# Optimization experiments

Measured on AMD Instinct MI355X. Metric: run time of the kernel, lower is better.

The kernel has to match this reference:

```python
import jax, jax.numpy as jnp
import numpy as np

B, S, I, H = 128, 512, 128, 512  # batch, seq_length(image_height), input_size(image_width), hidden(latent_dim)


def setup_inputs() -> dict:
    key = jax.random.key(0)
    ks = jax.random.split(key, 18)
    scale = 0.05

    def w(k, shape):
        return (jax.random.normal(k, shape, jnp.float32) * scale)

    inp = {"x": jax.random.normal(ks[0], (B, S, I), jnp.float32)}
    idx = 1
    for pre, in_sz in [("en0", I), ("en1", H), ("de0", I), ("de1", H)]:
        inp[f"W_ih_{pre}"] = w(ks[idx], (4 * H, in_sz)); idx += 1
        inp[f"W_hh_{pre}"] = w(ks[idx], (4 * H, H)); idx += 1
        inp[f"b_ih_{pre}"] = w(ks[idx], (4 * H,)); idx += 1
        inp[f"b_hh_{pre}"] = w(ks[idx], (4 * H,)); idx += 1
    inp["W_lin"] = w(ks[17], (I, H))  # nn.Linear(hidden, input, bias=False)
    return inp


def _cell(x, h, c, W_ih, W_hh, b_ih, b_hh):
    # PyTorch LSTM gate order: i, f, g, o
    gates = x @ W_ih.T + h @ W_hh.T + b_ih + b_hh
    i, f, g, o = jnp.split(gates, 4, axis=-1)
    c = jax.nn.sigmoid(f) * c + jax.nn.sigmoid(i) * jnp.tanh(g)
    h = jax.nn.sigmoid(o) * jnp.tanh(c)
    return h, c


def reference(x,
              W_ih_en0, W_hh_en0, b_ih_en0, b_hh_en0,
              W_ih_en1, W_hh_en1, b_ih_en1, b_hh_en1,
              W_ih_de0, W_hh_de0, b_ih_de0, b_hh_de0,
              W_ih_de1, W_hh_de1, b_ih_de1, b_hh_de1,
              W_lin):
    x = x.reshape((B, S, I))
    z = jnp.zeros((B, H), x.dtype)

    # ---- encoder: 2-layer LSTM, keep only final (hidden, cell) ----
    def enc_step(carry, xt):
        h0, c0, h1, c1 = carry
        h0, c0 = _cell(xt, h0, c0, W_ih_en0, W_hh_en0, b_ih_en0, b_hh_en0)
        h1, c1 = _cell(h0, h1, c1, W_ih_en1, W_hh_en1, b_ih_en1, b_hh_en1)
        return (h0, c0, h1, c1), None

    (h0, c0, h1, c1), _ = jax.lax.scan(enc_step, (z, z, z, z), jnp.swapaxes(x, 0, 1))

    # ---- decoder: closed-loop, feeding linear(output) back in ----
    def dec_step(carry, _):
        inp, h0, c0, h1, c1 = carry
        h0, c0 = _cell(inp, h0, c0, W_ih_de0, W_hh_de0, b_ih_de0, b_hh_de0)
        h1, c1 = _cell(h0, h1, c1, W_ih_de1, W_hh_de1, b_ih_de1, b_hh_de1)
        pred = h1 @ W_lin.T  # [B, I]
        return (pred, h0, c0, h1, c1), pred

    inp0 = jnp.zeros((B, I), x.dtype)
    _, preds = jax.lax.scan(dec_step, (inp0, h0, c0, h1, c1), None, length=S)
    return jnp.swapaxes(preds, 0, 1)  # [B, S, I]
```

## Files before the change

kernel.cpp:

```cpp
#include <hip/hip_runtime.h>
#include <hip/hip_fp16.h>


#define DEVINL __device__ __forceinline__

typedef _Float16 f16;
typedef _Float16 f16x8 __attribute__((ext_vector_type(8)));
typedef float    f32x4 __attribute__((ext_vector_type(4)));

constexpr int B = 128, S = 512, I = 128, H = 512, G4 = 4 * H;

constexpr size_t OFF_CNT    = 0;
constexpr size_t OFF_H1DBUF = 32768;
constexpr size_t OFF_C0     = 294912;
constexpr size_t OFF_C1     = 557056;
constexpr size_t OFF_H0ALL  = 819200;
constexpr size_t OFF_DDBUF  = 68059136;
constexpr size_t OFF_H1ST   = 68321280;
constexpr size_t OFF_XF16   = 135430144;
constexpr size_t OFF_WLIN16 = 152207360;
constexpr size_t OFF_BSUM   = 152338432;
constexpr size_t OFF_WEFF   = 152371200;
constexpr size_t ZERO_BYTES = 950272;

constexpr int LDS_L0   = 0;
constexpr int LDS_L1   = 40960;
constexpr int LDS_D0   = 0;
constexpr int LDS_D1   = 65536;
constexpr int LDS_SCR  = 131072;
constexpr int LDS_GB   = 146432;
constexpr int LDS_C0   = 150656;
constexpr int LDS_C1   = 151680;
constexpr int SMEM_BYTES = 152704;

DEVINL void cload(f16x8& r, const f16* p) {
    asm volatile("global_load_dwordx4 %0, %1, off sc0 sc1" : "=v"(r) : "v"(p));
}
DEVINL void ncload(f16x8& r, const f16* p) {
    asm volatile("global_load_dwordx4 %0, %1, off" : "=v"(r) : "v"(p));
}
DEVINL void cstore_h(f16* p, unsigned v) {
    asm volatile("global_store_short %0, %1, off sc0 sc1" :: "v"(p), "v"(v));
}
DEVINL void drain_vm() {
    asm volatile("s_waitcnt vmcnt(0)" ::: "memory");
    __builtin_amdgcn_sched_barrier(0);
}

__global__ void prep_kernel(const float* __restrict__ x,
                            const float* b0a, const float* b0b,
                            const float* b1a, const float* b1b,
                            const float* b2a, const float* b2b,
                            const float* b3a, const float* b3b,
                            const float* __restrict__ wlin, char* ws) {
    f16*   xf = (f16*)(ws + OFF_XF16);
    f16*   wl = (f16*)(ws + OFF_WLIN16);
    float* bs = (float*)(ws + OFF_BSUM);
    int tid = blockIdx.x * blockDim.x + threadIdx.x;
    int nth = gridDim.x * blockDim.x;
    for (int idx = tid; idx < S * B * I; idx += nth) {
        int i = idx & 127, b = (idx >> 7) & 127, t = idx >> 14;
        xf[idx] = (f16)x[((size_t)b * S + t) * I + i];
    }
    for (int idx = tid; idx < I * H; idx += nth) wl[idx] = (f16)wlin[idx];
    for (int idx = tid; idx < G4; idx += nth) {
        bs[idx]          = b0a[idx] + b0b[idx];
        bs[G4 + idx]     = b1a[idx] + b1b[idx];
        bs[2 * G4 + idx] = b2a[idx] + b2b[idx];
        bs[3 * G4 + idx] = b3a[idx] + b3b[idx];
    }
}

__global__ void weff_kernel(const float* __restrict__ wih_de0,
                            const float* __restrict__ wlin, char* ws) {
    float* weff = (float*)(ws + OFF_WEFF);
    int e  = blockIdx.x * 256 + threadIdx.x;
    int gc = e >> 9, k = e & 511;
    float acc = 0.f;
    for (int i = 0; i < I; ++i) acc += wih_de0[gc * I + i] * wlin[i * H + k];
    weff[e] = acc;
}

struct PParams {
    const float *wih0, *whh0, *wih1, *whh1, *whh2, *wih3, *whh3;
    char* ws;
};

DEVINL void wait2(unsigned* a, unsigned* b) {
    if (threadIdx.x == 0 && a)
        while (__hip_atomic_load(a, __ATOMIC_RELAXED, __HIP_MEMORY_SCOPE_AGENT) < 64u) {}
    if (threadIdx.x == 64 && b)
        while (__hip_atomic_load(b, __ATOMIC_RELAXED, __HIP_MEMORY_SCOPE_AGENT) < 64u) {}
    __syncthreads();
}

DEVINL void arrive(unsigned* c) {
    asm volatile("s_waitcnt vmcnt(0)" ::: "memory");
    __syncthreads();
    if (threadIdx.x == 0)
        __hip_atomic_fetch_add(c, 1u, __ATOMIC_RELAXED, __HIP_MEMORY_SCOPE_AGENT);
}

template <int K, int SPLIT>
DEVINL void fill_w(f16* ldsW, const float* __restrict__ matA,
                   const float* __restrict__ matB, int j0) {
    for (int idx = threadIdx.x; idx < 32 * K; idx += 512) {
        int c = idx / K, k = idx - c * K;
        int gcol = ((c >> 3) << 9) + j0 + (c & 7);
        float w = (k < SPLIT) ? matA[(size_t)gcol * SPLIT + k]
                              : matB[(size_t)gcol * (K - SPLIT) + (k - SPLIT)];
        int nt = c >> 4, lane = (((k >> 3) & 3) << 4) | (c & 15);
        int ks = k >> 5, j = k & 7;
        ldsW[(((size_t)nt * (K / 32) + ks) * 64 + lane) * 8 + j] = (f16)w;
    }
}

template <int K, int SPLIT, bool NCA>
DEVINL void lstm_round(const f16* __restrict__ actA, int strA,
                       const f16* __restrict__ actB, int strB, bool skipA,
                       const f16* __restrict__ ldsW, float biasN0, float biasN1,
                       float* scr, float* gb, float* c_lds,
                       f16* __restrict__ hdst, int m_idx, int j0) {
    const int tid = threadIdx.x;
    const int wv = tid >> 6, lane = tid & 63;
    const int m_t = wv >> 2, k_q = wv & 3;
    const int row = m_idx * 32 + m_t * 16 + (lane & 15);
    const int kk0 = (lane >> 4) * 8;
    constexpr int KS = K / 32;
    constexpr int SQ = KS / 4;
    const int ks0 = k_q * SQ;
    const f16* pa = actA + (size_t)row * strA + kk0;
    const f16* pb = actB + (size_t)row * strB + kk0 - SPLIT;

    f16x8 areg[SQ];
#pragma unroll
    for (int s = 0; s < SQ; ++s) {
        int kbase = (ks0 + s) * 32;
        if (kbase < SPLIT) {
            if (skipA) {
#pragma unroll
                for (int q = 0; q < 8; ++q) areg[s][q] = (f16)0;
            } else if (NCA) ncload(areg[s], pa + kbase);
            else            cload(areg[s], pa + kbase);
        } else cload(areg[s], pb + kbase);
    }
    drain_vm();

    f32x4 acc0 = (k_q == 0) ? (f32x4){biasN0, biasN0, biasN0, biasN0}
                            : (f32x4){0.f, 0.f, 0.f, 0.f};
    f32x4 acc1 = (k_q == 0) ? (f32x4){biasN1, biasN1, biasN1, biasN1}
                            : (f32x4){0.f, 0.f, 0.f, 0.f};
#pragma unroll
    for (int s = 0; s < SQ; ++s) {
        int ks = ks0 + s;
        f16x8 b0 = *(const f16x8*)(ldsW + (size_t)(ks * 64 + lane) * 8);
        f16x8 b1 = *(const f16x8*)(ldsW + (size_t)((KS + ks) * 64 + lane) * 8);
        acc0 = __builtin_amdgcn_mfma_f32_16x16x32_f16(areg[s], b0, acc0, 0, 0, 0);
        acc1 = __builtin_amdgcn_mfma_f32_16x16x32_f16(areg[s], b1, acc1, 0, 0, 0);
    }

    const int col = lane & 15, r0 = (lane >> 4) * 4;
    if (k_q) {
        *(f32x4*)(scr + ((m_t * 2 + 0) * 3 + (k_q - 1)) * 320 + col * 20 + r0) = acc0;
        *(f32x4*)(scr + ((m_t * 2 + 1) * 3 + (k_q - 1)) * 320 + col * 20 + r0) = acc1;
    }
    __syncthreads();
    if (k_q == 0) {
#pragma unroll
        for (int part = 0; part < 3; ++part) {
            acc0 += *(const f32x4*)(scr + ((m_t * 2 + 0) * 3 + part) * 320 + col * 20 + r0);
            acc1 += *(const f32x4*)(scr + ((m_t * 2 + 1) * 3 + part) * 320 + col * 20 + r0);
        }
#pragma unroll
        for (int i = 0; i < 4; ++i) {
            gb[(m_t * 16 + r0 + i) * 33 + col]      = acc0[i];
            gb[(m_t * 16 + r0 + i) * 33 + 16 + col] = acc1[i];
        }
    }
    __syncthreads();
    if (tid < 256) {
        int r = tid >> 3, jj = tid & 7;
        const float* grow = gb + r * 33;
        float gi = grow[jj], gf = grow[8 + jj], gg = grow[16 + jj], go = grow[24 + jj];
        float si = 1.f / (1.f + __expf(-gi));
        float sf = 1.f / (1.f + __expf(-gf));
        float so = 1.f / (1.f + __expf(-go));
        float tg = tanhf(gg);
        float cn = sf * c_lds[tid] + si * tg;
        c_lds[tid] = cn;
        union { f16 h; unsigned short u; } cvt;
        cvt.h = (f16)(so * tanhf(cn));
        cstore_h(hdst + (size_t)(m_idx * 32 + r) * H + j0 + jj, (unsigned)cvt.u);
    }
}

__global__ void __launch_bounds__(512, 1) lstm_persistent(PParams p) {
    extern __shared__ char smem[];
    char* ws = p.ws;
    unsigned* cnt = (unsigned*)(ws + OFF_CNT);
    f16*   h1db = (f16*)(ws + OFF_H1DBUF);
    f16*   h0all= (f16*)(ws + OFF_H0ALL);
    f16*   ddb  = (f16*)(ws + OFF_DDBUF);
    f16*   h1st = (f16*)(ws + OFF_H1ST);
    const f16*   xf   = (const f16*)(ws + OFF_XF16);
    const float* bs   = (const float*)(ws + OFF_BSUM);
    const float* weff = (const float*)(ws + OFF_WEFF);

    const int wg = blockIdx.x;
    const int m_idx = wg >> 6;
    const int n_idx = wg & 63;
    const int j0 = n_idx * 8;
    const int lane = threadIdx.x & 63;
    int c0col = lane & 15, c1col = 16 + (lane & 15);
    int g0 = ((c0col >> 3) << 9) + j0 + (c0col & 7);
    int g1 = ((c1col >> 3) << 9) + j0 + (c1col & 7);
    float b0n0 = bs[g0],          b0n1 = bs[g1];
    float b1n0 = bs[G4 + g0],     b1n1 = bs[G4 + g1];
    float b2n0 = bs[2 * G4 + g0], b2n1 = bs[2 * G4 + g1];
    float b3n0 = bs[3 * G4 + g0], b3n1 = bs[3 * G4 + g1];

    f16* ldsL0 = (f16*)(smem + LDS_L0);
    f16* ldsL1 = (f16*)(smem + LDS_L1);
    f16* ldsD0 = (f16*)(smem + LDS_D0);
    f16* ldsD1 = (f16*)(smem + LDS_D1);
    float* scr = (float*)(smem + LDS_SCR);
    float* gb  = (float*)(smem + LDS_GB);
    float* c0l = (float*)(smem + LDS_C0);
    float* c1l = (float*)(smem + LDS_C1);

    unsigned* cL0 = cnt;
    unsigned* cL1 = cnt + 512 * 4;
    unsigned* cD0 = cnt + 2 * 512 * 4;
    unsigned* cD1 = cnt + 3 * 512 * 4;

    if (threadIdx.x < 256) { c0l[threadIdx.x] = 0.f; c1l[threadIdx.x] = 0.f; }
    fill_w<640, 128>(ldsL0, p.wih0, p.whh0, j0);
    fill_w<1024, 512>(ldsL1, p.wih1, p.whh1, j0);
    __syncthreads();

    const int LAG = 3;
    for (int r = 0; r < 512 + LAG; ++r) {
        if (r < 512) {
            int t = r;
            wait2(t > 0 ? &cL0[(t - 1) * 4 + m_idx] : nullptr, nullptr);
            lstm_round<640, 128, true>(xf + (size_t)t * B * I, I,
                                       h0all + (size_t)t * B * H, H, false,
                                       ldsL0, b0n0, b0n1, scr, gb, c0l,
                                       h0all + (size_t)(t + 1) * B * H, m_idx, j0);
            arrive(&cL0[t * 4 + m_idx]);
        }
        if (r >= LAG) {
            int t = r - LAG;
            wait2(&cL0[t * 4 + m_idx],
                  t > 0 ? &cL1[(t - 1) * 4 + m_idx] : nullptr);
            lstm_round<1024, 512, false>(h0all + (size_t)(t + 1) * B * H, H,
                                         h1db + (size_t)((t - 1) & 1) * B * H, H, false,
                                         ldsL1, b1n0, b1n1, scr, gb, c1l,
                                         h1db + (size_t)(t & 1) * B * H, m_idx, j0);
            arrive(&cL1[t * 4 + m_idx]);
        }
    }

    __syncthreads();
    fill_w<1024, 512>(ldsD0, weff, p.whh2, j0);
    fill_w<1024, 512>(ldsD1, p.wih3, p.whh3, j0);
    __syncthreads();

    for (int t = 0; t < 512; ++t) {
        if (t == 0) wait2(&cL1[511 * 4 + m_idx], nullptr);
        else        wait2(&cD0[(t - 1) * 4 + m_idx], &cD1[(t - 1) * 4 + m_idx]);
        lstm_round<1024, 512, false>(
            t == 0 ? (h1db + (size_t)1 * B * H) : (h1st + (size_t)(t - 1) * B * H), H,
            t == 0 ? (h0all + (size_t)512 * B * H) : (ddb + (size_t)((t - 1) & 1) * B * H), H,
            t == 0,
            ldsD0, b2n0, b2n1, scr, gb, c0l,
            ddb + (size_t)(t & 1) * B * H, m_idx, j0);
        arrive(&cD0[t * 4 + m_idx]);

        wait2(&cD0[t * 4 + m_idx],
              t > 0 ? &cD1[(t - 1) * 4 + m_idx] : nullptr);
        lstm_round<1024, 512, false>(
            ddb + (size_t)(t & 1) * B * H, H,
            t == 0 ? (h1db + (size_t)1 * B * H) : (h1st + (size_t)(t - 1) * B * H), H,
            false,
            ldsD1, b3n0, b3n1, scr, gb, c1l,
            h1st + (size_t)t * B * H, m_idx, j0);
        arrive(&cD1[t * 4 + m_idx]);
    }
}

__global__ void __launch_bounds__(256) pred_kernel(const f16* __restrict__ h1s,
                                                   const f16* __restrict__ wl,
                                                   float* __restrict__ out) {
    int wg = blockIdx.x;
    int wv = threadIdx.x >> 6, lane = threadIdx.x & 63;
    int m0 = wg * 64 + wv * 16;
    int arow = m0 + (lane & 15);
    int kk0 = (lane >> 4) * 8;
    f32x4 acc[8];
#pragma unroll
    for (int n = 0; n < 8; ++n) acc[n] = (f32x4){0.f, 0.f, 0.f, 0.f};
#pragma unroll
    for (int ks = 0; ks < 16; ++ks) {
        f16x8 a = *(const f16x8*)(h1s + (size_t)arow * H + ks * 32 + kk0);
#pragma unroll
        for (int n = 0; n < 8; ++n) {
            f16x8 b = *(const f16x8*)(wl + (size_t)(n * 16 + (lane & 15)) * H + ks * 32 + kk0);
            acc[n] = __builtin_amdgcn_mfma_f32_16x16x32_f16(a, b, acc[n], 0, 0, 0);
        }
    }
    int col = lane & 15, r0 = (lane >> 4) * 4;
#pragma unroll
    for (int n = 0; n < 8; ++n)
#pragma unroll
        for (int i = 0; i < 4; ++i) {
            int m = m0 + r0 + i;
            int t = m >> 7, b = m & 127;
            out[((size_t)b * S + t) * I + n * 16 + col] = acc[n][i];
        }
}

extern "C" void kernel_launch(void* const* d_in, const int* in_sizes, int n_in,
                              void* d_out, int out_size, void* d_ws, size_t ws_size,
                              hipStream_t stream) {
    (void)in_sizes; (void)n_in; (void)out_size; (void)ws_size;
    const float* x        = (const float*)d_in[0];
    const float* wih_en0  = (const float*)d_in[1];
    const float* whh_en0  = (const float*)d_in[2];
    const float* bih_en0  = (const float*)d_in[3];
    const float* bhh_en0  = (const float*)d_in[4];
    const float* wih_en1  = (const float*)d_in[5];
    const float* whh_en1  = (const float*)d_in[6];
    const float* bih_en1  = (const float*)d_in[7];
    const float* bhh_en1  = (const float*)d_in[8];
    const float* wih_de0  = (const float*)d_in[9];
    const float* whh_de0  = (const float*)d_in[10];
    const float* bih_de0  = (const float*)d_in[11];
    const float* bhh_de0  = (const float*)d_in[12];
    const float* wih_de1  = (const float*)d_in[13];
    const float* whh_de1  = (const float*)d_in[14];
    const float* bih_de1  = (const float*)d_in[15];
    const float* bhh_de1  = (const float*)d_in[16];
    const float* wlin     = (const float*)d_in[17];
    char* ws = (char*)d_ws;

    hipMemsetAsync(ws, 0, ZERO_BYTES, stream);
    prep_kernel<<<2048, 256, 0, stream>>>(x, bih_en0, bhh_en0, bih_en1, bhh_en1,
                                          bih_de0, bhh_de0, bih_de1, bhh_de1,
                                          wlin, ws);
    weff_kernel<<<4096, 256, 0, stream>>>(wih_de0, wlin, ws);

    hipFuncSetAttribute((const void*)lstm_persistent,
                        hipFuncAttributeMaxDynamicSharedMemorySize, SMEM_BYTES);
    PParams p{wih_en0, whh_en0, wih_en1, whh_en1, whh_de0, wih_de1, whh_de1, ws};
    void* args[] = {&p};
    hipLaunchCooperativeKernel((const void*)lstm_persistent, dim3(256), dim3(512),
                               args, SMEM_BYTES, stream);

    pred_kernel<<<1024, 256, 0, stream>>>((const f16*)(ws + OFF_H1ST),
                                          (const f16*)(ws + OFF_WLIN16),
                                          (float*)d_out);
}
```

Measured before the change: 13.26 ms.

## Split encoder layers across dedicated workgroups and use per-block flag barriers

The encoder is restructured so the first 128 workgroups run layer 0 and the other 128 run layer 1 concurrently, each covering 64 rows with a 4x2 wave split, instead of every workgroup interleaving both layers with a fixed lag. The shared atomic counters are replaced by per-workgroup monotonic flags that a whole wavefront polls and checks with __all, and arrival becomes a plain store. Encoder cell states are handed to the decoder through global memory. Some activation loads switch from cache-bypassing asm to ordinary loads where the data was written earlier. This aims to cut serialisation and synchronisation latency in the recurrence, but it relies on those ordinary loads not returning stale cached data.

```diff
diff --git a/kernel.cpp b/kernel.cpp
--- a/kernel.cpp
+++ b/kernel.cpp
@@ -10,10 +10,10 @@
 
 constexpr int B = 128, S = 512, I = 128, H = 512, G4 = 4 * H;
 
-constexpr size_t OFF_CNT    = 0;
+constexpr size_t OFF_FLAGS  = 0;
 constexpr size_t OFF_H1DBUF = 32768;
-constexpr size_t OFF_C0     = 294912;
-constexpr size_t OFF_C1     = 557056;
+constexpr size_t OFF_C0G    = 294912;
+constexpr size_t OFF_C1G    = 557056;
 constexpr size_t OFF_H0ALL  = 819200;
 constexpr size_t OFF_DDBUF  = 68059136;
 constexpr size_t OFF_H1ST   = 68321280;
@@ -23,24 +23,25 @@
 constexpr size_t OFF_WEFF   = 152371200;
 constexpr size_t ZERO_BYTES = 950272;
 
-constexpr int LDS_L0   = 0;
-constexpr int LDS_L1   = 40960;
-constexpr int LDS_D0   = 0;
-constexpr int LDS_D1   = 65536;
+constexpr int LDS_W0   = 0;
+constexpr int LDS_W1   = 65536;
 constexpr int LDS_SCR  = 131072;
 constexpr int LDS_GB   = 146432;
-constexpr int LDS_C0   = 150656;
-constexpr int LDS_C1   = 151680;
-constexpr int SMEM_BYTES = 152704;
+constexpr int LDS_CA   = 154880;
+constexpr int LDS_CB   = 156928;
+constexpr int SMEM_BYTES = 158976;
 
 DEVINL void cload(f16x8& r, const f16* p) {
     asm volatile("global_load_dwordx4 %0, %1, off sc0 sc1" : "=v"(r) : "v"(p));
 }
-DEVINL void ncload(f16x8& r, const f16* p) {
-    asm volatile("global_load_dwordx4 %0, %1, off" : "=v"(r) : "v"(p));
+DEVINL void cload_f32(float& r, const float* p) {
+    asm volatile("global_load_dword %0, %1, off sc0 sc1" : "=v"(r) : "v"(p));
 }
 DEVINL void cstore_h(f16* p, unsigned v) {
     asm volatile("global_store_short %0, %1, off sc0 sc1" :: "v"(p), "v"(v));
+}
+DEVINL void cstore_f32(float* p, float v) {
+    asm volatile("global_store_dword %0, %1, off sc0 sc1" :: "v"(p), "v"(v));
 }
 DEVINL void drain_vm() {
     asm volatile("s_waitcnt vmcnt(0)" ::: "memory");
@@ -86,19 +87,30 @@
     char* ws;
 };
 
-DEVINL void wait2(unsigned* a, unsigned* b) {
-    if (threadIdx.x == 0 && a)
-        while (__hip_atomic_load(a, __ATOMIC_RELAXED, __HIP_MEMORY_SCOPE_AGENT) < 64u) {}
-    if (threadIdx.x == 64 && b)
-        while (__hip_atomic_load(b, __ATOMIC_RELAXED, __HIP_MEMORY_SCOPE_AGENT) < 64u) {}
-    __syncthreads();
-}
-
-DEVINL void arrive(unsigned* c) {
-    asm volatile("s_waitcnt vmcnt(0)" ::: "memory");
+DEVINL void waitA(const unsigned* f, unsigned tgt) {
+    if (f && threadIdx.x < 64) {
+        unsigned v;
+        do {
+            v = __hip_atomic_load(f + (threadIdx.x & 63),
+                                  __ATOMIC_RELAXED, __HIP_MEMORY_SCOPE_AGENT);
+        } while (!__all((int)(v >= tgt)));
+    }
+}
+DEVINL void waitB(const unsigned* f, unsigned tgt) {
+    if (f && threadIdx.x >= 64 && threadIdx.x < 128) {
+        unsigned v;
+        do {
+            v = __hip_atomic_load(f + (threadIdx.x & 63),
+                                  __ATOMIC_RELAXED, __HIP_MEMORY_SCOPE_AGENT);
+        } while (!__all((int)(v >= tgt)));
+    }
+}
+
+DEVINL void arrive(unsigned* f, unsigned val) {
+    drain_vm();
     __syncthreads();
     if (threadIdx.x == 0)
-        __hip_atomic_fetch_add(c, 1u, __ATOMIC_RELAXED, __HIP_MEMORY_SCOPE_AGENT);
+        __hip_atomic_store(f, val, __ATOMIC_RELAXED, __HIP_MEMORY_SCOPE_AGENT);
 }
 
 template <int K, int SPLIT>
@@ -115,20 +127,20 @@
     }
 }
 
-template <int K, int SPLIT, bool NCA>
+template <int K, int SPLIT, int MT, int KP, int AMODE, int BMODE>
 DEVINL void lstm_round(const f16* __restrict__ actA, int strA,
                        const f16* __restrict__ actB, int strB, bool skipA,
                        const f16* __restrict__ ldsW, float biasN0, float biasN1,
                        float* scr, float* gb, float* c_lds,
-                       f16* __restrict__ hdst, int m_idx, int j0) {
+                       f16* __restrict__ hdst, int row0, int j0) {
     const int tid = threadIdx.x;
     const int wv = tid >> 6, lane = tid & 63;
-    const int m_t = wv >> 2, k_q = wv & 3;
-    const int row = m_idx * 32 + m_t * 16 + (lane & 15);
+    const int m_t = wv / KP, k_p = wv % KP;
+    const int row = row0 + m_t * 16 + (lane & 15);
     const int kk0 = (lane >> 4) * 8;
     constexpr int KS = K / 32;
-    constexpr int SQ = KS / 4;
-    const int ks0 = k_q * SQ;
+    constexpr int SQ = KS / KP;
+    const int ks0 = k_p * SQ;
     const f16* pa = actA + (size_t)row * strA + kk0;
     const f16* pb = actB + (size_t)row * strB + kk0 - SPLIT;
 
@@ -140,15 +152,18 @@
             if (skipA) {
 #pragma unroll
                 for (int q = 0; q < 8; ++q) areg[s][q] = (f16)0;
-            } else if (NCA) ncload(areg[s], pa + kbase);
-            else            cload(areg[s], pa + kbase);
-        } else cload(areg[s], pb + kbase);
+            } else if (AMODE == 0) areg[s] = *(const f16x8*)(pa + kbase);
+            else                   cload(areg[s], pa + kbase);
+        } else {
+            if (BMODE == 0) areg[s] = *(const f16x8*)(pb + kbase);
+            else            cload(areg[s], pb + kbase);
+        }
     }
     drain_vm();
 
-    f32x4 acc0 = (k_q == 0) ? (f32x4){biasN0, biasN0, biasN0, biasN0}
+    f32x4 acc0 = (k_p == 0) ? (f32x4){biasN0, biasN0, biasN0, biasN0}
                             : (f32x4){0.f, 0.f, 0.f, 0.f};
-    f32x4 acc1 = (k_q == 0) ? (f32x4){biasN1, biasN1, biasN1, biasN1}
+    f32x4 acc1 = (k_p == 0) ? (f32x4){biasN1, biasN1, biasN1, biasN1}
                             : (f32x4){0.f, 0.f, 0.f, 0.f};
 #pragma unroll
     for (int s = 0; s < SQ; ++s) {
@@ -160,16 +175,16 @@
     }
 
     const int col = lane & 15, r0 = (lane >> 4) * 4;
-    if (k_q) {
-        *(f32x4*)(scr + ((m_t * 2 + 0) * 3 + (k_q - 1)) * 320 + col * 20 + r0) = acc0;
-        *(f32x4*)(scr + ((m_t * 2 + 1) * 3 + (k_q - 1)) * 320 + col * 20 + r0) = acc1;
-    }
-    __syncthreads();
-    if (k_q == 0) {
-#pragma unroll
-        for (int part = 0; part < 3; ++part) {
-            acc0 += *(const f32x4*)(scr + ((m_t * 2 + 0) * 3 + part) * 320 + col * 20 + r0);
-            acc1 += *(const f32x4*)(scr + ((m_t * 2 + 1) * 3 + part) * 320 + col * 20 + r0);
+    if (k_p) {
+        *(f32x4*)(scr + ((m_t * 2 + 0) * (KP - 1) + (k_p - 1)) * 320 + col * 20 + r0) = acc0;
+        *(f32x4*)(scr + ((m_t * 2 + 1) * (KP - 1) + (k_p - 1)) * 320 + col * 20 + r0) = acc1;
+    }
+    __syncthreads();
+    if (k_p == 0) {
+#pragma unroll
+        for (int part = 0; part < KP - 1; ++part) {
+            acc0 += *(const f32x4*)(scr + ((m_t * 2 + 0) * (KP - 1) + part) * 320 + col * 20 + r0);
+            acc1 += *(const f32x4*)(scr + ((m_t * 2 + 1) * (KP - 1) + part) * 320 + col * 20 + r0);
         }
 #pragma unroll
         for (int i = 0; i < 4; ++i) {
@@ -178,7 +193,7 @@
         }
     }
     __syncthreads();
-    if (tid < 256) {
+    if (tid < MT * 128) {
         int r = tid >> 3, jj = tid & 7;
         const float* grow = gb + r * 33;
         float gi = grow[jj], gf = grow[8 + jj], gg = grow[16 + jj], go = grow[24 + jj];
@@ -190,15 +205,21 @@
         c_lds[tid] = cn;
         union { f16 h; unsigned short u; } cvt;
         cvt.h = (f16)(so * tanhf(cn));
-        cstore_h(hdst + (size_t)(m_idx * 32 + r) * H + j0 + jj, (unsigned)cvt.u);
+        cstore_h(hdst + (size_t)(row0 + r) * H + j0 + jj, (unsigned)cvt.u);
     }
 }
 
 __global__ void __launch_bounds__(512, 1) lstm_persistent(PParams p) {
     extern __shared__ char smem[];
     char* ws = p.ws;
-    unsigned* cnt = (unsigned*)(ws + OFF_CNT);
+    unsigned* flg = (unsigned*)(ws + OFF_FLAGS);
+    unsigned* fL0 = flg;
+    unsigned* fL1 = flg + 128;
+    unsigned* fD0 = flg + 256;
+    unsigned* fD1 = flg + 512;
     f16*   h1db = (f16*)(ws + OFF_H1DBUF);
+    float* c0g  = (float*)(ws + OFF_C0G);
+    float* c1g  = (float*)(ws + OFF_C1G);
     f16*   h0all= (f16*)(ws + OFF_H0ALL);
     f16*   ddb  = (f16*)(ws + OFF_DDBUF);
     f16*   h1st = (f16*)(ws + OFF_H1ST);
@@ -207,10 +228,13 @@
     const float* weff = (const float*)(ws + OFF_WEFF);
 
     const int wg = blockIdx.x;
-    const int m_idx = wg >> 6;
+    const bool isL0 = wg < 128;
+    const int mh = (wg & 127) >> 6;
+    const int m  = wg >> 6;
     const int n_idx = wg & 63;
     const int j0 = n_idx * 8;
-    const int lane = threadIdx.x & 63;
+    const int tid = threadIdx.x, lane = tid & 63;
+
     int c0col = lane & 15, c1col = 16 + (lane & 15);
     int g0 = ((c0col >> 3) << 9) + j0 + (c0col & 7);
     int g1 = ((c1col >> 3) << 9) + j0 + (c1col & 7);
@@ -219,73 +243,98 @@
     float b2n0 = bs[2 * G4 + g0], b2n1 = bs[2 * G4 + g1];
     float b3n0 = bs[3 * G4 + g0], b3n1 = bs[3 * G4 + g1];
 
-    f16* ldsL0 = (f16*)(smem + LDS_L0);
-    f16* ldsL1 = (f16*)(smem + LDS_L1);
-    f16* ldsD0 = (f16*)(smem + LDS_D0);
-    f16* ldsD1 = (f16*)(smem + LDS_D1);
+    f16* ldsW0 = (f16*)(smem + LDS_W0);
+    f16* ldsW1 = (f16*)(smem + LDS_W1);
     float* scr = (float*)(smem + LDS_SCR);
     float* gb  = (float*)(smem + LDS_GB);
-    float* c0l = (float*)(smem + LDS_C0);
-    float* c1l = (float*)(smem + LDS_C1);
-
-    unsigned* cL0 = cnt;
-    unsigned* cL1 = cnt + 512 * 4;
-    unsigned* cD0 = cnt + 2 * 512 * 4;
-    unsigned* cD1 = cnt + 3 * 512 * 4;
-
-    if (threadIdx.x < 256) { c0l[threadIdx.x] = 0.f; c1l[threadIdx.x] = 0.f; }
-    fill_w<640, 128>(ldsL0, p.wih0, p.whh0, j0);
-    fill_w<1024, 512>(ldsL1, p.wih1, p.whh1, j0);
-    __syncthreads();
-
-    const int LAG = 3;
-    for (int r = 0; r < 512 + LAG; ++r) {
-        if (r < 512) {
-            int t = r;
-            wait2(t > 0 ? &cL0[(t - 1) * 4 + m_idx] : nullptr, nullptr);
-            lstm_round<640, 128, true>(xf + (size_t)t * B * I, I,
-                                       h0all + (size_t)t * B * H, H, false,
-                                       ldsL0, b0n0, b0n1, scr, gb, c0l,
-                                       h0all + (size_t)(t + 1) * B * H, m_idx, j0);
-            arrive(&cL0[t * 4 + m_idx]);
-        }
-        if (r >= LAG) {
-            int t = r - LAG;
-            wait2(&cL0[t * 4 + m_idx],
-                  t > 0 ? &cL1[(t - 1) * 4 + m_idx] : nullptr);
-            lstm_round<1024, 512, false>(h0all + (size_t)(t + 1) * B * H, H,
-                                         h1db + (size_t)((t - 1) & 1) * B * H, H, false,
-                                         ldsL1, b1n0, b1n1, scr, gb, c1l,
-                                         h1db + (size_t)(t & 1) * B * H, m_idx, j0);
-            arrive(&cL1[t * 4 + m_idx]);
-        }
-    }
-
-    __syncthreads();
-    fill_w<1024, 512>(ldsD0, weff, p.whh2, j0);
-    fill_w<1024, 512>(ldsD1, p.wih3, p.whh3, j0);
+    float* cA  = (float*)(smem + LDS_CA);
+    float* cB  = (float*)(smem + LDS_CB);
+
+    if (isL0) {
+        fill_w<640, 128>(ldsW0, p.wih0, p.whh0, j0);
+        cA[tid] = 0.f;
+        __syncthreads();
+        for (int t = 0; t < 512; ++t) {
+            waitA(t > 0 ? &fL0[mh * 64] : nullptr, (unsigned)t);
+            __syncthreads();
+            lstm_round<640, 128, 4, 2, 0, 0>(
+                xf + (size_t)t * B * I, I,
+                h0all + (size_t)t * B * H, H, false,
+                ldsW0, b0n0, b0n1, scr, gb, cA,
+                h0all + (size_t)(t + 1) * B * H, mh * 64, j0);
+            if (t == 511)
+                cstore_f32(&c0g[(size_t)(mh * 64 + (tid >> 3)) * H + j0 + (tid & 7)], cA[tid]);
+            arrive(&fL0[mh * 64 + n_idx], (unsigned)(t + 1));
+        }
+    } else {
+        fill_w<1024, 512>(ldsW0, p.wih1, p.whh1, j0);
+        cA[tid] = 0.f;
+        __syncthreads();
+        for (int t = 0; t < 512; ++t) {
+            waitA(&fL0[mh * 64], (unsigned)(t + 1));
+            waitB(t > 0 ? &fL1[mh * 64] : nullptr, (unsigned)t);
+            __syncthreads();
+            lstm_round<1024, 512, 4, 2, 0, 1>(
+                h0all + (size_t)(t + 1) * B * H, H,
+                h1db + (size_t)((t - 1) & 1) * B * H, H, false,
+                ldsW0, b1n0, b1n1, scr, gb, cA,
+                h1db + (size_t)(t & 1) * B * H, mh * 64, j0);
+            if (t == 511)
+                cstore_f32(&c1g[(size_t)(mh * 64 + (tid >> 3)) * H + j0 + (tid & 7)], cA[tid]);
+            arrive(&fL1[mh * 64 + n_idx], (unsigned)(t + 1));
+        }
+    }
+
+    __syncthreads();
+    fill_w<1024, 512>(ldsW0, weff, p.whh2, j0);
+    fill_w<1024, 512>(ldsW1, p.wih3, p.whh3, j0);
+    waitA(&fL0[(m >> 1) * 64], 512u);
+    waitB(&fL1[(m >> 1) * 64], 512u);
+    __syncthreads();
+    {
+        int r = (tid & 255) >> 3, jj = tid & 7;
+        float v;
+        cload_f32(v, (tid < 256 ? c0g : c1g) + (size_t)(m * 32 + r) * H + j0 + jj);
+        asm volatile("s_waitcnt vmcnt(0)" ::: "memory");
+        (tid < 256 ? cA : cB)[tid & 255] = v;
+    }
     __syncthreads();
 
     for (int t = 0; t < 512; ++t) {
-        if (t == 0) wait2(&cL1[511 * 4 + m_idx], nullptr);
-        else        wait2(&cD0[(t - 1) * 4 + m_idx], &cD1[(t - 1) * 4 + m_idx]);
-        lstm_round<1024, 512, false>(
-            t == 0 ? (h1db + (size_t)1 * B * H) : (h1st + (size_t)(t - 1) * B * H), H,
-            t == 0 ? (h0all + (size_t)512 * B * H) : (ddb + (size_t)((t - 1) & 1) * B * H), H,
-            t == 0,
-            ldsD0, b2n0, b2n1, scr, gb, c0l,
-            ddb + (size_t)(t & 1) * B * H, m_idx, j0);
-        arrive(&cD0[t * 4 + m_idx]);
-
-        wait2(&cD0[t * 4 + m_idx],
-              t > 0 ? &cD1[(t - 1) * 4 + m_idx] : nullptr);
-        lstm_round<1024, 512, false>(
-            ddb + (size_t)(t & 1) * B * H, H,
-            t == 0 ? (h1db + (size_t)1 * B * H) : (h1st + (size_t)(t - 1) * B * H), H,
-            false,
-            ldsD1, b3n0, b3n1, scr, gb, c1l,
-            h1st + (size_t)t * B * H, m_idx, j0);
-        arrive(&cD1[t * 4 + m_idx]);
+        if (t > 0) {
+            waitA(&fD0[m * 64], (unsigned)t);
+            waitB(&fD1[m * 64], (unsigned)t);
+            __syncthreads();
+        }
+        if (t == 0)
+            lstm_round<1024, 512, 2, 4, 0, 0>(
+                h1db, H,
+                h0all + (size_t)512 * B * H, H, true,
+                ldsW0, b2n0, b2n1, scr, gb, cA,
+                ddb, m * 32, j0);
+        else
+            lstm_round<1024, 512, 2, 4, 0, 1>(
+                h1st + (size_t)(t - 1) * B * H, H,
+                ddb + (size_t)((t - 1) & 1) * B * H, H, false,
+                ldsW0, b2n0, b2n1, scr, gb, cA,
+                ddb + (size_t)(t & 1) * B * H, m * 32, j0);
+        arrive(&fD0[m * 64 + n_idx], (unsigned)(t + 1));
+
+        waitA(&fD0[m * 64], (unsigned)(t + 1));
+        __syncthreads();
+        if (t == 0)
+            lstm_round<1024, 512, 2, 4, 1, 1>(
+                ddb, H,
+                h1db + (size_t)B * H, H, false,
+                ldsW1, b3n0, b3n1, scr, gb, cB,
+                h1st, m * 32, j0);
+        else
+            lstm_round<1024, 512, 2, 4, 1, 0>(
+                ddb + (size_t)(t & 1) * B * H, H,
+                h1st + (size_t)(t - 1) * B * H, H, false,
+                ldsW1, b3n0, b3n1, scr, gb, cB,
+                h1st + (size_t)t * B * H, m * 32, j0);
+        arrive(&fD1[m * 64 + n_idx], (unsigned)(t + 1));
     }
 }
 
@@ -314,8 +363,8 @@
     for (int n = 0; n < 8; ++n)
 #pragma unroll
         for (int i = 0; i < 4; ++i) {
-            int m = m0 + r0 + i;
-            int t = m >> 7, b = m & 127;
+            int mm = m0 + r0 + i;
+            int t = mm >> 7, b = mm & 127;
             out[((size_t)b * S + t) * I + n * 16 + col] = acc[n][i];
         }
 }
```

Measured after the change: 11.63 ms. 1.14x faster.
